# Kernel tuning notes

Hardware: AMD Instinct MI355X
Metric: run time of the kernel (lower is better)

Reference implementation:

```python
import jax, jax.numpy as jnp
import numpy as np

B, C, D = 65536, 10, 18
V, N, E = 100000, 99999, 128
EPS = 1e-9


def setup_inputs() -> dict:
    key = jax.random.key(0)
    k1, k2, k3, k4, k5 = jax.random.split(key, 5)
    return {
        "context_idxs": jax.random.randint(k1, (B, C), 0, V, dtype=jnp.int32),
        "path_nodes": jax.random.randint(k2, (B, D), 0, N, dtype=jnp.int32),
        "codes": jax.random.randint(k3, (B, D), 0, 2, dtype=jnp.int32),
        "in_embed": jax.random.normal(k4, (V, E), dtype=jnp.float32),
        "node_embed": jax.random.normal(k5, (N, E), dtype=jnp.float32),
    }


def reference(context_idxs, path_nodes, codes, in_embed, node_embed):
    # v: mean of context word embeddings -> [B, E]
    v = in_embed[context_idxs].mean(axis=1)
    # u: embeddings of internal tree nodes along the Huffman path -> [B, D, E]
    u = node_embed[path_nodes]
    # logits along the path: u . v -> [B, D]
    logits = jnp.einsum("bde,be->bd", u, v)
    s = jax.nn.sigmoid(logits)
    # p = s if code==1 else 1-s ; loss = -sum log(p + eps) per example
    p = jnp.where(codes == 1, s, 1.0 - s)
    loss = -jnp.sum(jnp.log(p + EPS), axis=1)  # [B]
    return loss
```

## Files before the change

### kernel.cpp

```cpp
#include <hip/hip_runtime.h>
#include <math.h>


constexpr int Bn = 65536;
constexpr int Cn = 10;
constexpr int Dn = 18;
constexpr int En = 128;
constexpr float EPS = 1e-9f;

__global__ __launch_bounds__(256) void cbow_hs_kernel(
    const int* __restrict__ ctx,
    const int* __restrict__ nodes,
    const int* __restrict__ codes,
    const float* __restrict__ in_embed,
    const float* __restrict__ node_embed,
    float* __restrict__ out)
{
    const int wave = threadIdx.x >> 6;
    const int lane = threadIdx.x & 63;
    const int b = (blockIdx.x << 2) + wave;

    const float2* __restrict__ in2 = (const float2*)in_embed;
    const float2* __restrict__ ne2 = (const float2*)node_embed;

    int cidx[Cn];
    #pragma unroll
    for (int c = 0; c < Cn; ++c) cidx[c] = ctx[b * Cn + c];

    float2 v = make_float2(0.f, 0.f);
    #pragma unroll
    for (int c = 0; c < Cn; ++c) {
        float2 e = in2[(size_t)cidx[c] * (En / 2) + lane];
        v.x += e.x;
        v.y += e.y;
    }
    v.x *= (1.0f / Cn);
    v.y *= (1.0f / Cn);

    int nidx[Dn], code[Dn];
    #pragma unroll
    for (int d = 0; d < Dn; ++d) {
        nidx[d] = nodes[b * Dn + d];
        code[d] = codes[b * Dn + d];
    }

    float pd[Dn];
    #pragma unroll
    for (int d = 0; d < Dn; ++d) {
        float2 u = ne2[(size_t)nidx[d] * (En / 2) + lane];
        pd[d] = u.x * v.x + u.y * v.y;
    }

    float loss = 0.f;
    #pragma unroll
    for (int d = 0; d < Dn; ++d) {
        float logit = pd[d];
        #pragma unroll
        for (int off = 32; off >= 1; off >>= 1)
            logit += __shfl_xor(logit, off, 64);
        float s = 1.0f / (1.0f + expf(-logit));
        float p = (code[d] == 1) ? s : 1.0f - s;
        loss -= logf(p + EPS);
    }

    if (lane == 0) out[b] = loss;
}

extern "C" void kernel_launch(void* const* d_in, const int* in_sizes, int n_in,
                              void* d_out, int out_size, void* d_ws, size_t ws_size,
                              hipStream_t stream) {
    const int*   ctx        = (const int*)d_in[0];
    const int*   path_nodes = (const int*)d_in[1];
    const int*   codes      = (const int*)d_in[2];
    const float* in_embed   = (const float*)d_in[3];
    const float* node_embed = (const float*)d_in[4];
    float*       out        = (float*)d_out;

    dim3 grid(Bn / 4);
    dim3 block(256);
    cbow_hs_kernel<<<grid, block, 0, stream>>>(ctx, path_nodes, codes,
                                               in_embed, node_embed, out);
}
```

Baseline: 239.6 us.

## Split wave into half-waves gathering two embedding rows each with float4 loads

Each 64-lane wave now handles two embedding rows at once. Each 32-lane half loads a full 128-float row using float4 (16-byte) loads instead of float2 across 64 lanes. Reductions shrink to 5 shuffle steps per pair of path nodes, and the sigmoid/log work is split across the two halves, so each lane does half as many transcendentals. Index loads are vectorized as int2. The intent is to cut the number of load instructions and shuffles per row. In exchange it adds some lane-select logic and a few cross-half shuffles.

```diff
diff --git a/kernel.cpp b/kernel.cpp
--- a/kernel.cpp
+++ b/kernel.cpp
@@ -5,7 +5,6 @@
 constexpr int Bn = 65536;
 constexpr int Cn = 10;
 constexpr int Dn = 18;
-constexpr int En = 128;
 constexpr float EPS = 1e-9f;
 
 __global__ __launch_bounds__(256) void cbow_hs_kernel(
@@ -18,50 +17,67 @@
 {
     const int wave = threadIdx.x >> 6;
     const int lane = threadIdx.x & 63;
+    const int sl   = lane & 31;
+    const bool hi  = lane >= 32;
     const int b = (blockIdx.x << 2) + wave;
 
-    const float2* __restrict__ in2 = (const float2*)in_embed;
-    const float2* __restrict__ ne2 = (const float2*)node_embed;
-
     int cidx[Cn];
+    const int2* c2 = (const int2*)(ctx + b * Cn);
     #pragma unroll
-    for (int c = 0; c < Cn; ++c) cidx[c] = ctx[b * Cn + c];
-
-    float2 v = make_float2(0.f, 0.f);
+    for (int k = 0; k < Cn / 2; ++k) {
+        int2 t = c2[k]; cidx[2 * k] = t.x; cidx[2 * k + 1] = t.y;
+    }
+    int nidx[Dn], code[Dn];
+    const int2* n2 = (const int2*)(nodes + b * Dn);
+    const int2* k2 = (const int2*)(codes + b * Dn);
     #pragma unroll
-    for (int c = 0; c < Cn; ++c) {
-        float2 e = in2[(size_t)cidx[c] * (En / 2) + lane];
-        v.x += e.x;
-        v.y += e.y;
-    }
-    v.x *= (1.0f / Cn);
-    v.y *= (1.0f / Cn);
-
-    int nidx[Dn], code[Dn];
-    #pragma unroll
-    for (int d = 0; d < Dn; ++d) {
-        nidx[d] = nodes[b * Dn + d];
-        code[d] = codes[b * Dn + d];
+    for (int k = 0; k < Dn / 2; ++k) {
+        int2 t = n2[k]; nidx[2 * k] = t.x; nidx[2 * k + 1] = t.y;
+        int2 u = k2[k]; code[2 * k] = u.x; code[2 * k + 1] = u.y;
     }
 
-    float pd[Dn];
+    const float4* __restrict__ in4 = (const float4*)in_embed;
+    const float4* __restrict__ ne4 = (const float4*)node_embed;
+
+    float4 vs = make_float4(0.f, 0.f, 0.f, 0.f);
     #pragma unroll
-    for (int d = 0; d < Dn; ++d) {
-        float2 u = ne2[(size_t)nidx[d] * (En / 2) + lane];
-        pd[d] = u.x * v.x + u.y * v.y;
+    for (int c = 0; c < Cn; c += 2) {
+        int idx = hi ? cidx[c + 1] : cidx[c];
+        float4 e = in4[(size_t)idx * 32 + sl];
+        vs.x += e.x; vs.y += e.y; vs.z += e.z; vs.w += e.w;
+    }
+    vs.x += __shfl_xor(vs.x, 32, 64);
+    vs.y += __shfl_xor(vs.y, 32, 64);
+    vs.z += __shfl_xor(vs.z, 32, 64);
+    vs.w += __shfl_xor(vs.w, 32, 64);
+    float4 v;
+    v.x = vs.x * (1.0f / Cn); v.y = vs.y * (1.0f / Cn);
+    v.z = vs.z * (1.0f / Cn); v.w = vs.w * (1.0f / Cn);
+
+    float pd[Dn / 2];
+    #pragma unroll
+    for (int i = 0; i < Dn / 2; ++i) {
+        int idx = hi ? nidx[2 * i + 1] : nidx[2 * i];
+        float4 u = ne4[(size_t)idx * 32 + sl];
+        pd[i] = u.x * v.x + u.y * v.y + u.z * v.z + u.w * v.w;
+    }
+
+    #pragma unroll
+    for (int i = 0; i < Dn / 2; ++i) {
+        #pragma unroll
+        for (int m = 16; m >= 1; m >>= 1)
+            pd[i] += __shfl_xor(pd[i], m, 64);
     }
 
     float loss = 0.f;
     #pragma unroll
-    for (int d = 0; d < Dn; ++d) {
-        float logit = pd[d];
-        #pragma unroll
-        for (int off = 32; off >= 1; off >>= 1)
-            logit += __shfl_xor(logit, off, 64);
-        float s = 1.0f / (1.0f + expf(-logit));
-        float p = (code[d] == 1) ? s : 1.0f - s;
+    for (int i = 0; i < Dn / 2; ++i) {
+        int cd = hi ? code[2 * i + 1] : code[2 * i];
+        float s = 1.0f / (1.0f + expf(-pd[i]));
+        float p = (cd == 1) ? s : 1.0f - s;
         loss -= logf(p + EPS);
     }
+    loss += __shfl_xor(loss, 32, 64);
 
     if (lane == 0) out[b] = loss;
 }
```

New measurement: 231.8 us. -3.3%, faster.
